# Optimization experiments

Measured on AMD Instinct MI355X. Metric: run time of the kernel, lower is better.

Reference implementation:

```python
import jax, jax.numpy as jnp
import numpy as np

K = 20          # top-k neighbors each side
C_THRESH = 0.0  # nnPU clipping threshold
GAMMA = 1.0
PRIOR_PRIME = 0.5


def _l2_normalize(x, eps=1e-12):
    # matches torch F.normalize(dim=1): x / max(||x||, eps)
    n = jnp.maximum(jnp.linalg.norm(x, axis=1, keepdims=True), eps)
    return x / n


def setup_inputs() -> dict:
    key = jax.random.key(0)
    k1, k2 = jax.random.split(key)
    N, C = 4096, 256
    return {
        "input": jax.random.normal(k1, (N, C), dtype=jnp.float32),
        "target": jax.random.normal(k2, (N, C), dtype=jnp.float32),
    }


def reference(input, target):
    pred_norm = _l2_normalize(input)      # [N, C]
    target_norm = _l2_normalize(target)   # [N, C]
    n = input.shape[0]

    # cosine distance in [0, 1]
    dist = (1.0 - pred_norm @ target_norm.T) * 0.5  # [N, N]

    eye = jnp.eye(n, dtype=bool)
    dist_ap = jnp.diagonal(dist)  # mask[i] selects only the diagonal -> max is dist[i,i]

    # off-diagonal top-k smallest / largest per row (mask diagonal with +/-inf)
    d_for_min = jnp.where(eye, jnp.inf, dist)
    d_for_max = jnp.where(eye, -jnp.inf, dist)
    neg_down_k, _ = jax.lax.top_k(-d_for_min, K)  # k smallest -> negated
    down_k = -neg_down_k                          # [N, K]
    up_k, _ = jax.lax.top_k(d_for_max, K)         # [N, K]

    sum_pos_unl = down_k.sum(axis=-1) + up_k.sum(axis=-1)  # [N]

    n_positive = 1.0
    n_unlabeled = 2.0 * K
    positive_risk = (PRIOR_PRIME / n_positive) * dist_ap
    negative_risk = -((1.0 - PRIOR_PRIME) / (n_positive * n_unlabeled)) * sum_pos_unl

    loss_i = jnp.where(negative_risk < C_THRESH,
                       -GAMMA * negative_risk,
                       positive_risk + negative_risk)
    return loss_i.mean()
```

## Files before the change

kernel.cpp:

```cpp
#include <hip/hip_runtime.h>
#include <hip/hip_bf16.h>
#include <math.h>

#define NROW 4096
#define CDIM 256
#define KSEL 20

typedef __attribute__((ext_vector_type(8))) short short8_t;
typedef __attribute__((ext_vector_type(4))) float f32x4;
typedef const __attribute__((address_space(1))) unsigned g_u32;
typedef __attribute__((address_space(3))) unsigned l_u32;

__device__ __forceinline__ unsigned sad_u8(unsigned a, unsigned b, unsigned c) {
    unsigned d;
    asm("v_sad_u8 %0, %1, %2, %3" : "=v"(d) : "v"(a), "v"(b), "v"(c));
    return d;
}

__global__ __launch_bounds__(256) void prep_kernel(const float* __restrict__ A,
                                                   const float* __restrict__ B,
                                                   ushort* __restrict__ An,
                                                   ushort* __restrict__ Bn) {
    const int tid  = threadIdx.x;
    const int lane = tid & 63;
    const int wid  = tid >> 6;
    const int r    = blockIdx.x * 4 + wid;
    const int row  = r & (NROW - 1);
    const float* __restrict__ X = (r < NROW) ? A : B;
    ushort* __restrict__ Y = (r < NROW) ? An : Bn;

    const float4 v = ((const float4*)(X + (size_t)row * CDIM))[lane];
    float s = v.x * v.x + v.y * v.y + v.z * v.z + v.w * v.w;
#pragma unroll
    for (int off = 32; off; off >>= 1) s += __shfl_xor(s, off, 64);
    const float rinv = 1.0f / fmaxf(sqrtf(s), 1e-12f);

    ushort4 o;
    __hip_bfloat16 h0 = __float2bfloat16(v.x * rinv); o.x = *(ushort*)&h0;
    __hip_bfloat16 h1 = __float2bfloat16(v.y * rinv); o.y = *(ushort*)&h1;
    __hip_bfloat16 h2 = __float2bfloat16(v.z * rinv); o.z = *(ushort*)&h2;
    __hip_bfloat16 h3 = __float2bfloat16(v.w * rinv); o.w = *(ushort*)&h3;
    ((ushort4*)(Y + (size_t)row * CDIM))[lane] = o;
}

__global__ __launch_bounds__(256) void gemm16_kernel(const ushort* __restrict__ An,
                                                     const ushort* __restrict__ Bn,
                                                     unsigned char* __restrict__ dist8) {
    const int tid  = threadIdx.x;
    const int lane = tid & 63;
    const int wid  = tid >> 6;
    const int wm = wid >> 1, wn = wid & 1;

    const int flat = blockIdx.x;
    const int wg   = (flat & 7) * 128 + (flat >> 3);
    const int j0   = (wg & 31) * 128;
    const int i0   = (wg >> 5) * 128;
    const int lr  = lane & 15;
    const int lk8 = (lane >> 4) * 8;

    __shared__ __align__(16) ushort As[2][4096];
    __shared__ __align__(16) ushort Bs[2][4096];

    const int srow = tid >> 2;
    const int scol = (tid & 3) * 8;
    const unsigned wbase = (unsigned)(wid * 1024);

    f32x4 acc[4][4];
#pragma unroll
    for (int m = 0; m < 4; ++m)
#pragma unroll
        for (int n = 0; n < 4; ++n) acc[m][n] = (f32x4){0.f, 0.f, 0.f, 0.f};

#pragma unroll
    for (int r = 0; r < 2; ++r) {
        const ushort* ga = An + (size_t)(i0 + r * 64 + srow) * CDIM + scol;
        __builtin_amdgcn_global_load_lds((g_u32*)ga,
            (l_u32*)((char*)As[0] + r * 4096 + wbase), 16, 0, 0);
        const ushort* gb = Bn + (size_t)(j0 + r * 64 + srow) * CDIM + scol;
        __builtin_amdgcn_global_load_lds((g_u32*)gb,
            (l_u32*)((char*)Bs[0] + r * 4096 + wbase), 16, 0, 0);
    }
    __syncthreads();

#pragma unroll
    for (int ks = 0; ks < 8; ++ks) {
        const int cur = ks & 1;
        if (ks < 7) {
            const int k0 = (ks + 1) * 32;
#pragma unroll
            for (int r = 0; r < 2; ++r) {
                const ushort* ga = An + (size_t)(i0 + r * 64 + srow) * CDIM + k0 + scol;
                __builtin_amdgcn_global_load_lds((g_u32*)ga,
                    (l_u32*)((char*)As[cur ^ 1] + r * 4096 + wbase), 16, 0, 0);
                const ushort* gb = Bn + (size_t)(j0 + r * 64 + srow) * CDIM + k0 + scol;
                __builtin_amdgcn_global_load_lds((g_u32*)gb,
                    (l_u32*)((char*)Bs[cur ^ 1] + r * 4096 + wbase), 16, 0, 0);
            }
        }
        {
            short8_t a[4], b[4];
#pragma unroll
            for (int m = 0; m < 4; ++m)
                a[m] = *(const short8_t*)&As[cur][(wm * 64 + m * 16 + lr) * 32 + lk8];
#pragma unroll
            for (int n = 0; n < 4; ++n)
                b[n] = *(const short8_t*)&Bs[cur][(wn * 64 + n * 16 + lr) * 32 + lk8];
#pragma unroll
            for (int m = 0; m < 4; ++m)
#pragma unroll
                for (int n = 0; n < 4; ++n)
                    acc[m][n] = __builtin_amdgcn_mfma_f32_16x16x32_bf16(a[m], b[n], acc[m][n], 0, 0, 0);
        }
        __syncthreads();
    }

    const int orow = (lane >> 4) * 4;
    const int ocol = lane & 15;
#pragma unroll
    for (int m = 0; m < 4; ++m)
#pragma unroll
        for (int q = 0; q < 4; ++q) {
            const int irow = i0 + wm * 64 + m * 16 + orow + q;
#pragma unroll
            for (int n = 0; n < 4; ++n) {
                float d = (1.0f - acc[m][n][q]) * 0.5f;
                d = fminf(fmaxf(d, 0.0f), 1.0f);
                unsigned key = __float2uint_rn(d * 127.0f);
                dist8[(size_t)irow * NROW + (j0 + wn * 64 + n * 16 + ocol)] = (unsigned char)key;
            }
        }
}

__global__ __launch_bounds__(256) void select_kernel(const unsigned char* __restrict__ dist8,
                                                     float* __restrict__ loss) {
    const int tid  = threadIdx.x;
    const int lane = tid & 63;
    const int wid  = tid >> 6;
    const int row  = blockIdx.x * 4 + wid;

    const uint4* __restrict__ P = (const uint4*)(dist8 + (size_t)row * NROW);
    unsigned w[16];
#pragma unroll
    for (int i = 0; i < 4; ++i) {
        uint4 v = P[i * 64 + lane];
        w[4 * i + 0] = v.x; w[4 * i + 1] = v.y;
        w[4 * i + 2] = v.z; w[4 * i + 3] = v.w;
    }
#pragma unroll
    for (int i = 0; i < 16; ++i) asm volatile("" : "+v"(w[i]));

    const unsigned dku = (unsigned)dist8[(size_t)row * NROW + row];
    const unsigned M = 0x80808080u;
    const unsigned zero = 0u;

    unsigned rs = 0;
#pragma unroll
    for (int i = 0; i < 16; ++i) rs = sad_u8(w[i], zero, rs);

    int lo1 = 0, hi1 = 128, clo = 0;
    int lo2 = -1, hi2 = 127, chi = 0;
#pragma unroll 1
    for (int it = 0; it < 7; ++it) {
        const int mid1 = (lo1 + hi1) >> 1;
        const int mid2 = (lo2 + hi2) >> 1;
        const unsigned C1 = (unsigned)(127 + mid1) * 0x01010101u;
        const unsigned C2 = (unsigned)(128 + mid2) * 0x01010101u;
        unsigned a1 = 0, a2 = 0;
#pragma unroll
        for (int i = 0; i < 16; ++i) {
            a1 = sad_u8((C1 - w[i]) & M, zero, a1);
            a2 = sad_u8((C2 - w[i]) & M, zero, a2);
        }
        int cc = (int)((a1 >> 7) | ((a2 >> 7) << 16));
#pragma unroll
        for (int off = 32; off; off >>= 1) cc += __shfl_xor(cc, off, 64);
        cc = __builtin_amdgcn_readfirstlane(cc);
        const int c1 = (cc & 0xFFFF) - ((dku < (unsigned)mid1) ? 1 : 0);
        const int c2 = (4096 - (cc >> 16)) - (((int)dku > mid2) ? 1 : 0);
        if (c1 < KSEL) { lo1 = mid1; clo = c1; } else hi1 = mid1;
        if (c2 < KSEL) { hi2 = mid2; chi = c2; } else lo2 = mid2;
    }
    const int Tmin = lo1, Tmax = hi2;

    const unsigned CA = (unsigned)(127 + Tmin) * 0x01010101u;
    const unsigned CB = (unsigned)(128 + Tmax) * 0x01010101u;
    unsigned sA = 0, sB = 0;
#pragma unroll
    for (int i = 0; i < 16; ++i) {
        const unsigned mA = ((CA - w[i]) & M) >> 7;
        sA = sad_u8(w[i] & ((mA << 8) - mA), zero, sA);
        const unsigned mB = ((CB - w[i]) & M) >> 7;
        sB = sad_u8(w[i] & ((mB << 8) - mB), zero, sB);
    }
#pragma unroll
    for (int off = 32; off; off >>= 1) {
        rs += __shfl_xor(rs, off, 64);
        sA += __shfl_xor(sA, off, 64);
        sB += __shfl_xor(sB, off, 64);
    }

    const int sum_min_i = (int)sA - ((dku < (unsigned)Tmin) ? (int)dku : 0)
                        + (KSEL - clo) * Tmin;
    const int sum_gt    = (int)(rs - sB);
    const int sum_max_i = sum_gt - (((int)dku > Tmax) ? (int)dku : 0)
                        + (KSEL - chi) * Tmax;

    if (lane == 0) {
        const float inv = 1.0f / 127.0f;
        const float total = (float)(sum_min_i + sum_max_i) * inv;
        const float dap = (float)dku * inv;
        const float neg = -0.0125f * total;
        const float pos = 0.5f * dap;
        loss[row] = (neg < 0.f) ? -neg : (pos + neg);
    }
}

__global__ __launch_bounds__(256) void finalize_kernel(const float* __restrict__ loss,
                                                       float* __restrict__ out) {
    const int tid = threadIdx.x;
    float s = 0.f;
    for (int k = tid; k < NROW; k += 256) s += loss[k];
#pragma unroll
    for (int off = 32; off; off >>= 1) s += __shfl_xor(s, off, 64);
    __shared__ float p[4];
    if ((tid & 63) == 0) p[tid >> 6] = s;
    __syncthreads();
    if (tid == 0) out[0] = (p[0] + p[1] + p[2] + p[3]) * (1.0f / (float)NROW);
}

extern "C" void kernel_launch(void* const* d_in, const int* in_sizes, int n_in,
                              void* d_out, int out_size, void* d_ws, size_t ws_size,
                              hipStream_t stream) {
    const float* A = (const float*)d_in[0];
    const float* B = (const float*)d_in[1];

    char* ws = (char*)d_ws;
    const size_t norm_bytes = (size_t)NROW * CDIM * 2;
    ushort* An = (ushort*)ws;
    ushort* Bn = (ushort*)(ws + norm_bytes);
    float*  lossv = (float*)(ws + 2 * norm_bytes);
    unsigned char* dist8 = (unsigned char*)(ws + 2 * norm_bytes + (size_t)NROW * 4);
    float* outp = (float*)d_out;

    prep_kernel<<<2 * NROW / 4, 256, 0, stream>>>(A, B, An, Bn);
    gemm16_kernel<<<1024, 256, 0, stream>>>(An, Bn, dist8);
    select_kernel<<<NROW / 4, 256, 0, stream>>>(dist8, lossv);
    finalize_kernel<<<1, 256, 0, stream>>>(lossv, outp);
}
```

Before: 45.16 us.

## Fuse L2 normalization into GEMM by scaling dot products with row norms

Removes the separate prep kernel that normalized rows and wrote bf16 copies. The GEMM now loads raw fp32 rows, converts them to bf16 in registers, writes them to LDS and accumulates sum-of-squares along the way. Row inverse norms are applied to the dot products in the epilogue. This saves a kernel launch and the bf16 round trip through memory, but the GEMM now reads twice the bytes of fp32 input, loses the async global_load_lds path, and rounds un-normalized values to bf16.

```diff
diff --git a/kernel.cpp b/kernel.cpp
--- a/kernel.cpp
+++ b/kernel.cpp
@@ -8,8 +8,6 @@
 
 typedef __attribute__((ext_vector_type(8))) short short8_t;
 typedef __attribute__((ext_vector_type(4))) float f32x4;
-typedef const __attribute__((address_space(1))) unsigned g_u32;
-typedef __attribute__((address_space(3))) unsigned l_u32;
 
 __device__ __forceinline__ unsigned sad_u8(unsigned a, unsigned b, unsigned c) {
     unsigned d;
@@ -17,35 +15,25 @@
     return d;
 }
 
-__global__ __launch_bounds__(256) void prep_kernel(const float* __restrict__ A,
-                                                   const float* __restrict__ B,
-                                                   ushort* __restrict__ An,
-                                                   ushort* __restrict__ Bn) {
-    const int tid  = threadIdx.x;
-    const int lane = tid & 63;
-    const int wid  = tid >> 6;
-    const int r    = blockIdx.x * 4 + wid;
-    const int row  = r & (NROW - 1);
-    const float* __restrict__ X = (r < NROW) ? A : B;
-    ushort* __restrict__ Y = (r < NROW) ? An : Bn;
-
-    const float4 v = ((const float4*)(X + (size_t)row * CDIM))[lane];
-    float s = v.x * v.x + v.y * v.y + v.z * v.z + v.w * v.w;
-#pragma unroll
-    for (int off = 32; off; off >>= 1) s += __shfl_xor(s, off, 64);
-    const float rinv = 1.0f / fmaxf(sqrtf(s), 1e-12f);
-
-    ushort4 o;
-    __hip_bfloat16 h0 = __float2bfloat16(v.x * rinv); o.x = *(ushort*)&h0;
-    __hip_bfloat16 h1 = __float2bfloat16(v.y * rinv); o.y = *(ushort*)&h1;
-    __hip_bfloat16 h2 = __float2bfloat16(v.z * rinv); o.z = *(ushort*)&h2;
-    __hip_bfloat16 h3 = __float2bfloat16(v.w * rinv); o.w = *(ushort*)&h3;
-    ((ushort4*)(Y + (size_t)row * CDIM))[lane] = o;
-}
-
-__global__ __launch_bounds__(256) void gemm16_kernel(const ushort* __restrict__ An,
-                                                     const ushort* __restrict__ Bn,
-                                                     unsigned char* __restrict__ dist8) {
+__device__ __forceinline__ void cvt_store(ushort* dst, float4 x, float4 y, float& ssq) {
+    ssq += x.x * x.x + x.y * x.y + x.z * x.z + x.w * x.w
+         + y.x * y.x + y.y * y.y + y.z * y.z + y.w * y.w;
+    union { ushort u[8]; short8_t v; } p;
+    __hip_bfloat16 h;
+    h = __float2bfloat16(x.x); p.u[0] = *(ushort*)&h;
+    h = __float2bfloat16(x.y); p.u[1] = *(ushort*)&h;
+    h = __float2bfloat16(x.z); p.u[2] = *(ushort*)&h;
+    h = __float2bfloat16(x.w); p.u[3] = *(ushort*)&h;
+    h = __float2bfloat16(y.x); p.u[4] = *(ushort*)&h;
+    h = __float2bfloat16(y.y); p.u[5] = *(ushort*)&h;
+    h = __float2bfloat16(y.z); p.u[6] = *(ushort*)&h;
+    h = __float2bfloat16(y.w); p.u[7] = *(ushort*)&h;
+    *(short8_t*)dst = p.v;
+}
+
+__global__ __launch_bounds__(256, 3) void gemmn_kernel(const float* __restrict__ A,
+                                                       const float* __restrict__ B,
+                                                       unsigned char* __restrict__ dist8) {
     const int tid  = threadIdx.x;
     const int lane = tid & 63;
     const int wid  = tid >> 6;
@@ -60,10 +48,17 @@
 
     __shared__ __align__(16) ushort As[2][4096];
     __shared__ __align__(16) ushort Bs[2][4096];
+    __shared__ float rinvA[128], rinvB[128];
 
     const int srow = tid >> 2;
     const int scol = (tid & 3) * 8;
-    const unsigned wbase = (unsigned)(wid * 1024);
+    const float* __restrict__ ga0 = A + (size_t)(i0 + srow) * CDIM + scol;
+    const float* __restrict__ ga1 = A + (size_t)(i0 + 64 + srow) * CDIM + scol;
+    const float* __restrict__ gb0 = B + (size_t)(j0 + srow) * CDIM + scol;
+    const float* __restrict__ gb1 = B + (size_t)(j0 + 64 + srow) * CDIM + scol;
+
+    float ssa0 = 0.f, ssa1 = 0.f, ssb0 = 0.f, ssb1 = 0.f;
+    float4 la0a, la0b, la1a, la1b, lb0a, lb0b, lb1a, lb1b;
 
     f32x4 acc[4][4];
 #pragma unroll
@@ -71,32 +66,30 @@
 #pragma unroll
         for (int n = 0; n < 4; ++n) acc[m][n] = (f32x4){0.f, 0.f, 0.f, 0.f};
 
-#pragma unroll
-    for (int r = 0; r < 2; ++r) {
-        const ushort* ga = An + (size_t)(i0 + r * 64 + srow) * CDIM + scol;
-        __builtin_amdgcn_global_load_lds((g_u32*)ga,
-            (l_u32*)((char*)As[0] + r * 4096 + wbase), 16, 0, 0);
-        const ushort* gb = Bn + (size_t)(j0 + r * 64 + srow) * CDIM + scol;
-        __builtin_amdgcn_global_load_lds((g_u32*)gb,
-            (l_u32*)((char*)Bs[0] + r * 4096 + wbase), 16, 0, 0);
-    }
+#define STAGE_LOAD(K0)                                                        \
+    {                                                                         \
+        la0a = *(const float4*)(ga0 + (K0));  la0b = *(const float4*)(ga0 + (K0) + 4); \
+        la1a = *(const float4*)(ga1 + (K0));  la1b = *(const float4*)(ga1 + (K0) + 4); \
+        lb0a = *(const float4*)(gb0 + (K0));  lb0b = *(const float4*)(gb0 + (K0) + 4); \
+        lb1a = *(const float4*)(gb1 + (K0));  lb1b = *(const float4*)(gb1 + (K0) + 4); \
+    }
+
+#define STAGE_WRITE(BUF)                                                      \
+    {                                                                         \
+        cvt_store(&As[BUF][srow * 32 + scol],        la0a, la0b, ssa0);       \
+        cvt_store(&As[BUF][(64 + srow) * 32 + scol], la1a, la1b, ssa1);       \
+        cvt_store(&Bs[BUF][srow * 32 + scol],        lb0a, lb0b, ssb0);       \
+        cvt_store(&Bs[BUF][(64 + srow) * 32 + scol], lb1a, lb1b, ssb1);       \
+    }
+
+    STAGE_LOAD(0);
+    STAGE_WRITE(0);
     __syncthreads();
 
 #pragma unroll
     for (int ks = 0; ks < 8; ++ks) {
         const int cur = ks & 1;
-        if (ks < 7) {
-            const int k0 = (ks + 1) * 32;
-#pragma unroll
-            for (int r = 0; r < 2; ++r) {
-                const ushort* ga = An + (size_t)(i0 + r * 64 + srow) * CDIM + k0 + scol;
-                __builtin_amdgcn_global_load_lds((g_u32*)ga,
-                    (l_u32*)((char*)As[cur ^ 1] + r * 4096 + wbase), 16, 0, 0);
-                const ushort* gb = Bn + (size_t)(j0 + r * 64 + srow) * CDIM + k0 + scol;
-                __builtin_amdgcn_global_load_lds((g_u32*)gb,
-                    (l_u32*)((char*)Bs[cur ^ 1] + r * 4096 + wbase), 16, 0, 0);
-            }
-        }
+        if (ks < 7) STAGE_LOAD((ks + 1) * 32);
         {
             short8_t a[4], b[4];
 #pragma unroll
@@ -111,24 +104,43 @@
                 for (int n = 0; n < 4; ++n)
                     acc[m][n] = __builtin_amdgcn_mfma_f32_16x16x32_bf16(a[m], b[n], acc[m][n], 0, 0, 0);
         }
+        if (ks < 7) STAGE_WRITE(cur ^ 1);
         __syncthreads();
     }
+
+    ssa0 += __shfl_xor(ssa0, 1, 64); ssa0 += __shfl_xor(ssa0, 2, 64);
+    ssa1 += __shfl_xor(ssa1, 1, 64); ssa1 += __shfl_xor(ssa1, 2, 64);
+    ssb0 += __shfl_xor(ssb0, 1, 64); ssb0 += __shfl_xor(ssb0, 2, 64);
+    ssb1 += __shfl_xor(ssb1, 1, 64); ssb1 += __shfl_xor(ssb1, 2, 64);
+    if ((tid & 3) == 0) {
+        rinvA[srow]      = 1.0f / fmaxf(sqrtf(ssa0), 1e-12f);
+        rinvA[64 + srow] = 1.0f / fmaxf(sqrtf(ssa1), 1e-12f);
+        rinvB[srow]      = 1.0f / fmaxf(sqrtf(ssb0), 1e-12f);
+        rinvB[64 + srow] = 1.0f / fmaxf(sqrtf(ssb1), 1e-12f);
+    }
+    __syncthreads();
 
     const int orow = (lane >> 4) * 4;
     const int ocol = lane & 15;
+    float rb[4];
+#pragma unroll
+    for (int n = 0; n < 4; ++n) rb[n] = rinvB[wn * 64 + n * 16 + ocol];
 #pragma unroll
     for (int m = 0; m < 4; ++m)
 #pragma unroll
         for (int q = 0; q < 4; ++q) {
-            const int irow = i0 + wm * 64 + m * 16 + orow + q;
+            const int irow = wm * 64 + m * 16 + orow + q;
+            const float ra = rinvA[irow];
 #pragma unroll
             for (int n = 0; n < 4; ++n) {
-                float d = (1.0f - acc[m][n][q]) * 0.5f;
+                float d = (1.0f - acc[m][n][q] * ra * rb[n]) * 0.5f;
                 d = fminf(fmaxf(d, 0.0f), 1.0f);
                 unsigned key = __float2uint_rn(d * 127.0f);
-                dist8[(size_t)irow * NROW + (j0 + wn * 64 + n * 16 + ocol)] = (unsigned char)key;
+                dist8[(size_t)(i0 + irow) * NROW + (j0 + wn * 64 + n * 16 + ocol)] = (unsigned char)key;
             }
         }
+#undef STAGE_LOAD
+#undef STAGE_WRITE
 }
 
 __global__ __launch_bounds__(256) void select_kernel(const unsigned char* __restrict__ dist8,
@@ -235,15 +247,11 @@
     const float* B = (const float*)d_in[1];
 
     char* ws = (char*)d_ws;
-    const size_t norm_bytes = (size_t)NROW * CDIM * 2;
-    ushort* An = (ushort*)ws;
-    ushort* Bn = (ushort*)(ws + norm_bytes);
-    float*  lossv = (float*)(ws + 2 * norm_bytes);
-    unsigned char* dist8 = (unsigned char*)(ws + 2 * norm_bytes + (size_t)NROW * 4);
+    float* lossv = (float*)ws;
+    unsigned char* dist8 = (unsigned char*)(ws + (size_t)NROW * 4);
     float* outp = (float*)d_out;
 
-    prep_kernel<<<2 * NROW / 4, 256, 0, stream>>>(A, B, An, Bn);
-    gemm16_kernel<<<1024, 256, 0, stream>>>(An, Bn, dist8);
+    gemmn_kernel<<<1024, 256, 0, stream>>>(A, B, dist8);
     select_kernel<<<NROW / 4, 256, 0, stream>>>(dist8, lossv);
     finalize_kernel<<<1, 256, 0, stream>>>(lossv, outp);
 }
```

Result: slower. 57.16 us (+26.6%).
